# Performance work log

Hardware: AMD Instinct MI355X
Metric: run time of the kernel (lower is better)

## Reference

```python
import jax, jax.numpy as jnp
import numpy as np
from jax import lax

STRIDE = (1, 1)
PADDING = ((1, 1), (1, 1))  # padding=1 for 3x3 kernel -> same spatial size


def _conv_one(xi, wi, bi):
    # xi: [C_in, H, W], wi: [C_out, C_in, k, k], bi: [C_out]
    out = lax.conv_general_dilated(
        xi[None], wi, window_strides=STRIDE, padding=PADDING,
        dimension_numbers=('NCHW', 'OIHW', 'NCHW'))
    return out[0] + bi[:, None, None]


def setup_inputs() -> dict:
    key = jax.random.key(0)
    k1, k2, k3, k4 = jax.random.split(key, 4)
    B, C_in, H, W = 16, 64, 128, 128
    C_out, K, ks = 64, 5, 3
    x = jax.random.normal(k1, (B, C_in, H, W), dtype=jnp.float32)
    weights = jax.random.uniform(k2, (B, K), dtype=jnp.float32)  # attention over K kernels
    Wbank = jax.random.normal(k3, (K, C_out, C_in, ks, ks), dtype=jnp.float32)
    bbank = jax.random.normal(k4, (K, C_out), dtype=jnp.float32) * 0.1
    return {"x": x, "weights": weights, "Wbank": Wbank, "bbank": bbank}


def reference(x, weights, Wbank, bbank):
    # Per-sample aggregated kernels: [B, C_out, C_in, k, k]
    agg_w = jnp.einsum('bk,koihw->boihw', weights, Wbank)
    # Per-sample aggregated bias: [B, C_out]
    agg_b = weights @ bbank
    # Grouped conv with groups = batch, expressed as vmapped per-sample conv
    return jax.vmap(_conv_one)(x, agg_w, agg_b)
```

## Files before the change

kernel.cpp:

```cpp
#include <hip/hip_runtime.h>
#include <hip/hip_bf16.h>


typedef __attribute__((ext_vector_type(8))) __bf16 bf16x8;
typedef __attribute__((ext_vector_type(16))) float f32x16;
typedef __attribute__((ext_vector_type(4))) unsigned int u32x4;

#define NB 16
#define CI 64
#define CO 64
#define HH 128
#define WW 128
#define KBANK 5
#define ASTR 36864

__device__ __forceinline__ unsigned short f2bfu(float f) {
    __hip_bfloat16 h = __float2bfloat16(f);
    unsigned short s;
    __builtin_memcpy(&s, &h, 2);
    return s;
}

__global__ void prep_kernel(const float* __restrict__ weights,
                            const float* __restrict__ Wbank,
                            const float* __restrict__ bbank,
                            short* __restrict__ aggw,
                            float* __restrict__ aggb) {
    int idx = blockIdx.x * 256 + threadIdx.x;
    int b   = idx / ASTR;
    int rem = idx - b * ASTR;
    int j   = rem & 7;
    int co5 = (rem >> 3) & 31;
    int g   = (rem >> 8) & 1;
    int mk  = rem >> 9;
    int m   = mk / 36;
    int ks  = mk - m * 36;
    int co  = m * 32 + co5;
    int k   = ks * 16 + g * 8 + j;
    int tap = k >> 6;
    int ci  = k & 63;
    float s = 0.f;
#pragma unroll
    for (int kk = 0; kk < KBANK; ++kk)
        s += weights[b * KBANK + kk] * Wbank[((kk * CO + co) * CI + ci) * 9 + tap];
    aggw[idx] = (short)f2bfu(s);
    if (k == 0) {
        float sb = 0.f;
#pragma unroll
        for (int kk = 0; kk < KBANK; ++kk)
            sb += weights[b * KBANK + kk] * bbank[kk * CO + co];
        aggb[b * CO + co] = sb;
    }
}

#define WAITV(N) asm volatile("s_waitcnt vmcnt(" #N ")" ::: "memory")
#define WAITL0   asm volatile("s_waitcnt lgkmcnt(0)" ::: "memory")
#define SBAR     do { __builtin_amdgcn_s_barrier(); __builtin_amdgcn_sched_barrier(0); } while (0)

__global__ __launch_bounds__(512, 2) void conv_kernel(const float* __restrict__ x,
                                                      const short* __restrict__ aggw,
                                                      const float* __restrict__ aggb,
                                                      float* __restrict__ out) {
    __shared__ short bring[4][8][130][8];
    __shared__ float fring[2][64][128];

    const int t   = threadIdx.x;
    const int lin = blockIdx.x;
    const int b   = (lin & 7) * 2 + ((lin >> 3) & 1);
    const int r0  = (lin >> 4) * 8;

    const int l  = t & 63;
    const int wv = t >> 6;
    const int m  = wv >> 2;
    const int nq = wv & 3;
    const int lm = l & 31;
    const int g  = l >> 5;

    const float* xb = x + (size_t)b * CI * HH * WW;
    const short* Ab = aggw + (size_t)b * ASTR + (size_t)m * 36 * 512;

    bf16x8 A[36];
#pragma unroll
    for (int ks = 0; ks < 36; ++ks)
        A[ks] = *(const bf16x8*)(Ab + ks * 512 + l * 8);

    float bias[16];
#pragma unroll
    for (int rg = 0; rg < 16; ++rg)
        bias[rg] = aggb[b * CO + m * 32 + (rg & 3) + 8 * (rg >> 2) + 4 * g];

    if (t < 64) {
        int slot = t >> 4, ch = (t >> 1) & 7, px = (t & 1) * 129;
        *(u32x4*)&bring[slot][ch][px][0] = u32x4{0u, 0u, 0u, 0u};
    }

    auto stage = [&](int r, int fs) {
        float* fbase = &fring[fs][0][0];
#pragma unroll
        for (int i = 0; i < 4; ++i) {
            int c  = i * 512 + t;
            int ci = c >> 5;
            int w  = (c & 31) * 4;
            const float* src = xb + ((size_t)ci * HH + r) * WW + w;
            float* dst = fbase + (size_t)(i * 512 + (t & ~63)) * 4;
            __builtin_amdgcn_global_load_lds(
                (const __attribute__((address_space(1))) void*)src,
                (__attribute__((address_space(3))) void*)dst, 16, 0, 0);
        }
    };

    auto convertz = [&](const float* fbase, int bs, bool zero) {
#pragma unroll
        for (int k2 = 0; k2 < 2; ++k2) {
            int c   = k2 * 512 + t;
            int ch  = c >> 7;
            int pix = (c & 127) + 1;
            unsigned u0 = 0, u1 = 0, u2 = 0, u3 = 0;
            if (!zero) {
                const float* p = fbase + ch * 1024 + (pix - 1);
                u0 = (unsigned)f2bfu(p[0])   | ((unsigned)f2bfu(p[128]) << 16);
                u1 = (unsigned)f2bfu(p[256]) | ((unsigned)f2bfu(p[384]) << 16);
                u2 = (unsigned)f2bfu(p[512]) | ((unsigned)f2bfu(p[640]) << 16);
                u3 = (unsigned)f2bfu(p[768]) | ((unsigned)f2bfu(p[896]) << 16);
            }
            *(u32x4*)&bring[bs][ch][pix][0] = u32x4{u0, u1, u2, u3};
        }
    };

    if (r0 > 0) stage(r0 - 1, 1);
    stage(r0, 0);
    WAITV(4); SBAR;
    if (r0 > 0) convertz(&fring[1][0][0], 0, false);
    else        convertz(nullptr,         0, true);
    WAITV(0);
    WAITL0; SBAR;
    convertz(&fring[0][0][0], 1, false);
    stage(r0 + 1, 1);
    WAITL0; SBAR;
    WAITV(0); SBAR;
    convertz(&fring[1][0][0], 2, false);
    stage(r0 + 2, 0);
    WAITL0; SBAR;

#pragma unroll
    for (int s = 0; s < 8; ++s) {
        const int r = r0 + s;

        if (s == 0) { WAITV(0); } else { WAITV(16); }
        SBAR;

        if (s <= 6) {
            if (r + 2 <= 127) convertz(&fring[s & 1][0][0], (s + 3) & 3, false);
            else              convertz(nullptr,             (s + 3) & 3, true);
        }

        if (s <= 5 && r + 3 <= 127) stage(r + 3, (s + 1) & 1);

        f32x16 acc = (f32x16)0.0f;
#pragma unroll
        for (int ks = 0; ks < 36; ++ks) {
            const int tap = ks >> 2, q = ks & 3;
            const int dy = tap / 3, dx = tap - dy * 3;
            const short* sb = &bring[(s + dy) & 3][0][0][0];
            const int pix = nq * 32 + dx + lm;
            bf16x8 bv = *(const bf16x8*)&sb[((q * 2 + g) * 130 + pix) * 8];
            acc = __builtin_amdgcn_mfma_f32_32x32x16_bf16(A[ks], bv, acc, 0, 0, 0);
        }

        const int wc = nq * 32 + lm;
#pragma unroll
        for (int rg = 0; rg < 16; ++rg) {
            int co = m * 32 + (rg & 3) + 8 * (rg >> 2) + 4 * g;
            out[(((size_t)b * CO + co) * HH + r) * WW + wc] = acc[rg] + bias[rg];
        }

        WAITL0;
        SBAR;
    }
}

extern "C" void kernel_launch(void* const* d_in, const int* in_sizes, int n_in,
                              void* d_out, int out_size, void* d_ws, size_t ws_size,
                              hipStream_t stream) {
    const float* x       = (const float*)d_in[0];
    const float* weights = (const float*)d_in[1];
    const float* Wbank   = (const float*)d_in[2];
    const float* bbank   = (const float*)d_in[3];
    float* out = (float*)d_out;

    short* aggw = (short*)d_ws;
    float* aggb = (float*)((char*)d_ws + 1179648);

    prep_kernel<<<dim3((NB * ASTR) / 256), dim3(256), 0, stream>>>(weights, Wbank, bbank, aggw, aggb);
    conv_kernel<<<dim3(256), dim3(512), 0, stream>>>(x, aggw, aggb, out);
}
```

Measured before the change: 39.88 us.

## Split conv block into producer and consumer warp groups

Dedicates four waves to staging input rows into LDS and converting them to bf16, while the other four waves run the MFMA loop, each computing two 32-pixel tiles with a shared A fragment. The aim is to overlap global loads and conversion with matrix math and to halve A-register loading across waves. The cost is that only half the waves issue MFMAs, and the per-row barrier synchronisation now couples the two groups, so the slower group sets the pace.

Result: slower. 49.72 us (+24.7%).

```diff
diff --git a/kernel.cpp b/kernel.cpp
--- a/kernel.cpp
+++ b/kernel.cpp
@@ -71,30 +71,34 @@
 
     const int l  = t & 63;
     const int wv = t >> 6;
-    const int m  = wv >> 2;
-    const int nq = wv & 3;
+    const bool is_prod = (wv >= 4);
+    const int pt = t & 255;
+
+    const int m  = (wv >> 1) & 1;
+    const int nh = wv & 1;
     const int lm = l & 31;
     const int g  = l >> 5;
 
     const float* xb = x + (size_t)b * CI * HH * WW;
-    const short* Ab = aggw + (size_t)b * ASTR + (size_t)m * 36 * 512;
 
     bf16x8 A[36];
-#pragma unroll
-    for (int ks = 0; ks < 36; ++ks)
-        A[ks] = *(const bf16x8*)(Ab + ks * 512 + l * 8);
-
     float bias[16];
-#pragma unroll
-    for (int rg = 0; rg < 16; ++rg)
-        bias[rg] = aggb[b * CO + m * 32 + (rg & 3) + 8 * (rg >> 2) + 4 * g];
+    if (!is_prod) {
+        const short* Ab = aggw + (size_t)b * ASTR + (size_t)m * 36 * 512;
+#pragma unroll
+        for (int ks = 0; ks < 36; ++ks)
+            A[ks] = *(const bf16x8*)(Ab + ks * 512 + l * 8);
+#pragma unroll
+        for (int rg = 0; rg < 16; ++rg)
+            bias[rg] = aggb[b * CO + m * 32 + (rg & 3) + 8 * (rg >> 2) + 4 * g];
+    }
 
     if (t < 64) {
         int slot = t >> 4, ch = (t >> 1) & 7, px = (t & 1) * 129;
         *(u32x4*)&bring[slot][ch][px][0] = u32x4{0u, 0u, 0u, 0u};
     }
 
-    auto stage = [&](int r, int fs) {
+    auto stageAll = [&](int r, int fs) {
         float* fbase = &fring[fs][0][0];
 #pragma unroll
         for (int i = 0; i < 4; ++i) {
@@ -102,14 +106,27 @@
             int ci = c >> 5;
             int w  = (c & 31) * 4;
             const float* src = xb + ((size_t)ci * HH + r) * WW + w;
-            float* dst = fbase + (size_t)(i * 512 + (t & ~63)) * 4;
+            float* dst = fbase + (size_t)c * 4;
             __builtin_amdgcn_global_load_lds(
                 (const __attribute__((address_space(1))) void*)src,
                 (__attribute__((address_space(3))) void*)dst, 16, 0, 0);
         }
     };
-
-    auto convertz = [&](const float* fbase, int bs, bool zero) {
+    auto stageProd = [&](int r, int fs) {
+        float* fbase = &fring[fs][0][0];
+#pragma unroll
+        for (int i = 0; i < 8; ++i) {
+            int c  = i * 256 + pt;
+            int ci = c >> 5;
+            int w  = (c & 31) * 4;
+            const float* src = xb + ((size_t)ci * HH + r) * WW + w;
+            float* dst = fbase + (size_t)c * 4;
+            __builtin_amdgcn_global_load_lds(
+                (const __attribute__((address_space(1))) void*)src,
+                (__attribute__((address_space(3))) void*)dst, 16, 0, 0);
+        }
+    };
+    auto convAll = [&](const float* fbase, int bs, bool zero) {
 #pragma unroll
         for (int k2 = 0; k2 < 2; ++k2) {
             int c   = k2 * 512 + t;
@@ -126,52 +143,77 @@
             *(u32x4*)&bring[bs][ch][pix][0] = u32x4{u0, u1, u2, u3};
         }
     };
-
-    if (r0 > 0) stage(r0 - 1, 1);
-    stage(r0, 0);
+    auto convProd = [&](const float* fbase, int bs, bool zero) {
+#pragma unroll
+        for (int k2 = 0; k2 < 4; ++k2) {
+            int c   = k2 * 256 + pt;
+            int ch  = c >> 7;
+            int pix = (c & 127) + 1;
+            unsigned u0 = 0, u1 = 0, u2 = 0, u3 = 0;
+            if (!zero) {
+                const float* p = fbase + ch * 1024 + (pix - 1);
+                u0 = (unsigned)f2bfu(p[0])   | ((unsigned)f2bfu(p[128]) << 16);
+                u1 = (unsigned)f2bfu(p[256]) | ((unsigned)f2bfu(p[384]) << 16);
+                u2 = (unsigned)f2bfu(p[512]) | ((unsigned)f2bfu(p[640]) << 16);
+                u3 = (unsigned)f2bfu(p[768]) | ((unsigned)f2bfu(p[896]) << 16);
+            }
+            *(u32x4*)&bring[bs][ch][pix][0] = u32x4{u0, u1, u2, u3};
+        }
+    };
+
+    if (r0 > 0) stageAll(r0 - 1, 1);
+    stageAll(r0, 0);
     WAITV(4); SBAR;
-    if (r0 > 0) convertz(&fring[1][0][0], 0, false);
-    else        convertz(nullptr,         0, true);
+    if (r0 > 0) convAll(&fring[1][0][0], 0, false);
+    else        convAll(nullptr,         0, true);
     WAITV(0);
     WAITL0; SBAR;
-    convertz(&fring[0][0][0], 1, false);
-    stage(r0 + 1, 1);
+    convAll(&fring[0][0][0], 1, false);
+    stageAll(r0 + 1, 1);
     WAITL0; SBAR;
     WAITV(0); SBAR;
-    convertz(&fring[1][0][0], 2, false);
-    stage(r0 + 2, 0);
+    convAll(&fring[1][0][0], 2, false);
+    if (is_prod) stageProd(r0 + 2, 0);
     WAITL0; SBAR;
 
 #pragma unroll
     for (int s = 0; s < 8; ++s) {
         const int r = r0 + s;
 
-        if (s == 0) { WAITV(0); } else { WAITV(16); }
+        if (is_prod && s <= 6) { WAITV(0); }
         SBAR;
 
-        if (s <= 6) {
-            if (r + 2 <= 127) convertz(&fring[s & 1][0][0], (s + 3) & 3, false);
-            else              convertz(nullptr,             (s + 3) & 3, true);
-        }
-
-        if (s <= 5 && r + 3 <= 127) stage(r + 3, (s + 1) & 1);
-
-        f32x16 acc = (f32x16)0.0f;
-#pragma unroll
-        for (int ks = 0; ks < 36; ++ks) {
-            const int tap = ks >> 2, q = ks & 3;
-            const int dy = tap / 3, dx = tap - dy * 3;
-            const short* sb = &bring[(s + dy) & 3][0][0][0];
-            const int pix = nq * 32 + dx + lm;
-            bf16x8 bv = *(const bf16x8*)&sb[((q * 2 + g) * 130 + pix) * 8];
-            acc = __builtin_amdgcn_mfma_f32_32x32x16_bf16(A[ks], bv, acc, 0, 0, 0);
-        }
-
-        const int wc = nq * 32 + lm;
-#pragma unroll
-        for (int rg = 0; rg < 16; ++rg) {
-            int co = m * 32 + (rg & 3) + 8 * (rg >> 2) + 4 * g;
-            out[(((size_t)b * CO + co) * HH + r) * WW + wc] = acc[rg] + bias[rg];
+        if (is_prod) {
+            if (s <= 6) {
+                if (r + 2 <= 127) convProd(&fring[s & 1][0][0], (s + 3) & 3, false);
+                else              convProd(nullptr,             (s + 3) & 3, true);
+            }
+            if (s <= 5 && r + 3 <= 127) stageProd(r + 3, (s + 1) & 1);
+        } else {
+            f32x16 accA = (f32x16)0.0f;
+            f32x16 accB = (f32x16)0.0f;
+#pragma unroll
+            for (int ks = 0; ks < 36; ++ks) {
+                const int tap = ks >> 2, q = ks & 3;
+                const int dy = tap / 3, dx = tap - dy * 3;
+                const short* sb = &bring[(s + dy) & 3][0][0][0];
+                const int pixA = nh * 64 + lm + dx;
+                bf16x8 bvA = *(const bf16x8*)&sb[((q * 2 + g) * 130 + pixA) * 8];
+                bf16x8 bvB = *(const bf16x8*)&sb[((q * 2 + g) * 130 + pixA + 32) * 8];
+                accA = __builtin_amdgcn_mfma_f32_32x32x16_bf16(A[ks], bvA, accA, 0, 0, 0);
+                accB = __builtin_amdgcn_mfma_f32_32x32x16_bf16(A[ks], bvB, accB, 0, 0, 0);
+            }
+            const int wcA = nh * 64 + lm;
+#pragma unroll
+            for (int rg = 0; rg < 16; ++rg) {
+                int co = m * 32 + (rg & 3) + 8 * (rg >> 2) + 4 * g;
+                out[(((size_t)b * CO + co) * HH + r) * WW + wcA] = accA[rg] + bias[rg];
+            }
+#pragma unroll
+            for (int rg = 0; rg < 16; ++rg) {
+                int co = m * 32 + (rg & 3) + 8 * (rg >> 2) + 4 * g;
+                out[(((size_t)b * CO + co) * HH + r) * WW + wcA + 32] = accB[rg] + bias[rg];
+            }
         }
 
         WAITL0;
```
